# Kernel tuning notes

Hardware: AMD Instinct MI355X
Metric: run time of the kernel (lower is better)

Reference implementation:

```python
import jax, jax.numpy as jnp
import numpy as np

N_WORD = 50000
N_DOC = 10000
E_WW = 800000
E_WD = 320000


def _sage(h_src, h_dst, src, dst, n_dst, W_self, W_neigh, b):
    # DGL SAGEConv('mean'): fc_self(h_dst) + fc_neigh(mean_{u in N(v)} h_u) + bias
    ones = jnp.ones((src.shape[0],), dtype=h_src.dtype)
    deg = jax.ops.segment_sum(ones, dst, num_segments=n_dst)            # [n_dst]
    agg = jax.ops.segment_sum(h_src[src], dst, num_segments=n_dst)      # [n_dst, d]
    mean = agg / jnp.maximum(deg, 1.0)[:, None]                          # zero for isolated
    return h_dst @ W_self + mean @ W_neigh + b


def _layer(xw, xd, edges, Ws, Wn, b):
    (ww_s, ww_d, wwr_s, wwr_d, wd_s, wd_d, wdr_s, wdr_d) = edges
    # relations targeting 'word': word2word, word2wordr, word2documentr
    h_ww = _sage(xw, xw, ww_s, ww_d, N_WORD, Ws[0], Wn[0], b[0])
    h_wwr = _sage(xw, xw, wwr_s, wwr_d, N_WORD, Ws[1], Wn[1], b[1])
    h_wdr = _sage(xd, xw, wdr_s, wdr_d, N_WORD, Ws[3], Wn[3], b[3])
    # relation targeting 'document': word2document
    h_wd = _sage(xw, xd, wd_s, wd_d, N_DOC, Ws[2], Wn[2], b[2])
    # HeteroGraphConv aggregate='stack' then torch.sum(dim=1) == sum over relations; then relu
    return jax.nn.relu(h_ww + h_wwr + h_wdr), jax.nn.relu(h_wd)


def setup_inputs() -> dict:
    key = jax.random.key(0)
    ks = jax.random.split(key, 20)
    d_in, d_h = 256, 128
    inp = {
        "x_word": jax.random.normal(ks[0], (N_WORD, d_in), jnp.float32),
        "x_doc": jax.random.normal(ks[1], (N_DOC, d_in), jnp.float32),
        "ww_src": jax.random.randint(ks[2], (E_WW,), 0, N_WORD, jnp.int32),
        "ww_dst": jax.random.randint(ks[3], (E_WW,), 0, N_WORD, jnp.int32),
        "wwr_src": jax.random.randint(ks[4], (E_WW,), 0, N_WORD, jnp.int32),
        "wwr_dst": jax.random.randint(ks[5], (E_WW,), 0, N_WORD, jnp.int32),
        "wd_src": jax.random.randint(ks[6], (E_WD,), 0, N_WORD, jnp.int32),
        "wd_dst": jax.random.randint(ks[7], (E_WD,), 0, N_DOC, jnp.int32),
        "wdr_src": jax.random.randint(ks[8], (E_WD,), 0, N_DOC, jnp.int32),
        "wdr_dst": jax.random.randint(ks[9], (E_WD,), 0, N_WORD, jnp.int32),
        "Wself1": jax.random.normal(ks[10], (4, d_in, d_h), jnp.float32) * (1.0 / np.sqrt(d_in)),
        "Wneigh1": jax.random.normal(ks[11], (4, d_in, d_h), jnp.float32) * (1.0 / np.sqrt(d_in)),
        "b1": jnp.zeros((4, d_h), jnp.float32),
        "Wself2": jax.random.normal(ks[12], (4, d_h, d_h), jnp.float32) * (1.0 / np.sqrt(d_h)),
        "Wneigh2": jax.random.normal(ks[13], (4, d_h, d_h), jnp.float32) * (1.0 / np.sqrt(d_h)),
        "b2": jnp.zeros((4, d_h), jnp.float32),
        "lin_w": jax.random.normal(ks[14], (1, d_h), jnp.float32) * (1.0 / np.sqrt(d_h)),
        "lin_b": jnp.ones((1,), jnp.float32),
    }
    return inp


def reference(x_word, x_doc, ww_src, ww_dst, wwr_src, wwr_dst, wd_src, wd_dst,
              wdr_src, wdr_dst, Wself1, Wneigh1, b1, Wself2, Wneigh2, b2, lin_w, lin_b):
    edges = (ww_src, ww_dst, wwr_src, wwr_dst, wd_src, wd_dst, wdr_src, wdr_dst)
    xw, xd = _layer(x_word, x_doc, edges, Wself1, Wneigh1, b1)
    xw, xd = _layer(xw, xd, edges, Wself2, Wneigh2, b2)
    out_w = jax.nn.sigmoid(xw @ lin_w.T + lin_b)  # [N_WORD, 1]
    out_d = jax.nn.sigmoid(xd @ lin_w.T + lin_b)  # [N_DOC, 1]
    return out_w, out_d
```

## Files before the change

kernel.cpp:

```cpp
#include <hip/hip_runtime.h>
#include <math.h>

#define N_WORD 50000
#define N_DOC  10000
#define E_WW   800000
#define E_WD   320000
#define D_IN   256
#define D_H    128

#define NPB    256
#define NBK_W  196
#define NBK_D  40
#define BKT    (3 * NBK_W + NBK_D)
#define EPB    8192
#define NBLK_WW 98
#define NBLK_WD 40
#define NBLK_TOT (2 * NBLK_WW + 2 * NBLK_WD)
#define PACK_BLKS 145

#define CAP_WW  4736
#define CAP_WDR 2176
#define CAP_WD  8960

#define WSTRIP ((N_WORD + 63) / 64)
#define DSTRIP ((N_DOC + 63) / 64)
#define NSTRIP (WSTRIP + DSTRIP)

typedef __attribute__((ext_vector_type(8))) short short8;
typedef __attribute__((ext_vector_type(4))) float f32x4;

__device__ inline unsigned short f2bf(float f) {
  unsigned u = __float_as_uint(f);
  u = (u + 0x7fffu + ((u >> 16) & 1u)) >> 16;
  return (unsigned short)u;
}

struct G6 { const short* B[6]; unsigned short* C[6]; };

template <int ABF, int K>
__device__ void gemm_body(const void* __restrict__ Aw, const void* __restrict__ Ad,
                          const G6& g, int blk) {
  constexpr int KT = K >> 5;
  int wid = threadIdx.x >> 6, lane = threadIdx.x & 63;
  const void* A; int M, row0, h0, h1;
  if (blk < WSTRIP) { A = Aw; M = N_WORD; row0 = blk << 6; h0 = 0; h1 = 4; }
  else { A = Ad; M = N_DOC; row0 = (blk - WSTRIP) << 6; h0 = 4; h1 = 6; }
  int r = lane & 15, quad = lane >> 4;
  int m0 = row0 + wid * 16;
  int mA = m0 + r; if (mA >= M) mA = M - 1;
  short8 afr[KT];
  if (ABF) {
    const short* ap = (const short*)A + (size_t)mA * K + quad * 8;
#pragma unroll
    for (int kt = 0; kt < KT; ++kt) afr[kt] = *(const short8*)(ap + kt * 32);
  } else {
    const float* ap = (const float*)A + (size_t)mA * K + quad * 8;
#pragma unroll
    for (int kt = 0; kt < KT; ++kt) {
      float4 a0 = *(const float4*)(ap + kt * 32);
      float4 a1 = *(const float4*)(ap + kt * 32 + 4);
      short8 v;
      v[0] = (short)f2bf(a0.x); v[1] = (short)f2bf(a0.y);
      v[2] = (short)f2bf(a0.z); v[3] = (short)f2bf(a0.w);
      v[4] = (short)f2bf(a1.x); v[5] = (short)f2bf(a1.y);
      v[6] = (short)f2bf(a1.z); v[7] = (short)f2bf(a1.w);
      afr[kt] = v;
    }
  }
  for (int h = h0; h < h1; ++h) {
    const short* Bp = g.B[h];
    f32x4 acc[8];
#pragma unroll
    for (int nt = 0; nt < 8; ++nt) acc[nt] = (f32x4){0.f, 0.f, 0.f, 0.f};
#pragma unroll
    for (int kt = 0; kt < KT; ++kt) {
      const short* bbase = Bp + ((size_t)kt * 4096) + lane * 8;
#pragma unroll
      for (int nt = 0; nt < 8; ++nt) {
        short8 bf = *(const short8*)(bbase + (size_t)nt * 512);
        acc[nt] = __builtin_amdgcn_mfma_f32_16x16x32_bf16(afr[kt], bf, acc[nt], 0, 0, 0);
      }
    }
    unsigned short* C = g.C[h];
#pragma unroll
    for (int nt = 0; nt < 8; ++nt)
#pragma unroll
      for (int rr = 0; rr < 4; ++rr) {
        int row = m0 + quad * 4 + rr;
        if (row < M) C[(size_t)row * 128 + nt * 16 + r] = f2bf(acc[nt][rr]);
      }
  }
}

__global__ __launch_bounds__(256) void prep_kernel(
    const float* __restrict__ Ws1, const float* __restrict__ Wn1,
    const float* __restrict__ Ws2, const float* __restrict__ Wn2,
    short* __restrict__ Bp1, short* __restrict__ Bp2,
    const float* __restrict__ b1, const float* __restrict__ b2,
    float* __restrict__ bs1, float* __restrict__ bs2, int* __restrict__ bcnt) {
  int b = blockIdx.x;
  if (b == PACK_BLKS) {
    for (int i = threadIdx.x; i < BKT; i += 256) bcnt[i] = 0;
    return;
  }
  int tid = b * 256 + threadIdx.x;
  const int L1T = 6 * 4096;
  const int L2T = 6 * 2048;
  if (tid >= L1T + L2T) {
    int t = tid - (L1T + L2T);
    if (t < 128) bs1[t] = b1[t] + b1[128 + t] + b1[384 + t];
    else if (t < 256) { int u = t - 128; bs2[u] = b2[u] + b2[128 + u] + b2[384 + u]; }
    return;
  }
  const float *src0, *src1 = nullptr, *src2 = nullptr;
  short* dstp;
  int kt, nt, lane;
  if (tid < L1T) {
    int mat = tid / 4096, rem = tid % 4096;
    kt = rem / 512; nt = (rem / 64) % 8; lane = rem % 64;
    const int W1 = 256 * 128;
    if (mat == 0) { src0 = Ws1; src1 = Ws1 + W1; src2 = Ws1 + 3 * W1; }
    else if (mat <= 4) src0 = Wn1 + (size_t)(mat - 1) * W1;
    else src0 = Ws1 + 2 * W1;
    dstp = Bp1 + (size_t)mat * W1 + ((size_t)(kt * 8 + nt) * 64 + lane) * 8;
  } else {
    int t2 = tid - L1T;
    int mat = t2 / 2048, rem = t2 % 2048;
    kt = rem / 512; nt = (rem / 64) % 8; lane = rem % 64;
    const int W2 = 128 * 128;
    if (mat == 0) { src0 = Ws2; src1 = Ws2 + W2; src2 = Ws2 + 3 * W2; }
    else if (mat <= 4) src0 = Wn2 + (size_t)(mat - 1) * W2;
    else src0 = Ws2 + 2 * W2;
    dstp = Bp2 + (size_t)mat * W2 + ((size_t)(kt * 8 + nt) * 64 + lane) * 8;
  }
  int n = nt * 16 + (lane & 15);
  int kb = kt * 32 + (lane >> 4) * 8;
  short8 v;
#pragma unroll
  for (int j = 0; j < 8; ++j) {
    float f = src0[(size_t)(kb + j) * 128 + n];
    if (src1) f += src1[(size_t)(kb + j) * 128 + n] + src2[(size_t)(kb + j) * 128 + n];
    v[j] = (short)f2bf(f);
  }
  *(short8*)dstp = v;
}

__device__ inline void rel_map(int b, const int* wwd, const int* wwrd, const int* wdrd,
                               const int* wdd, const int*& dst, int& E, int& gbase, int& lb) {
  if (b < NBLK_WW) { dst = wwd; E = E_WW; gbase = 0; lb = b; }
  else if (b < 2 * NBLK_WW) { dst = wwrd; E = E_WW; gbase = NBK_W; lb = b - NBLK_WW; }
  else if (b < 2 * NBLK_WW + NBLK_WD) { dst = wdrd; E = E_WD; gbase = 2 * NBK_W; lb = b - 2 * NBLK_WW; }
  else { dst = wdd; E = E_WD; gbase = 3 * NBK_W; lb = b - 2 * NBLK_WW - NBLK_WD; }
}

struct BinLDS {
  unsigned buf[EPB];
  int hist[NBK_W];
  int lofs[NBK_W];
  int gofs[NBK_W];
  int lcur[NBK_W];
  int sm[256];
};

__global__ __launch_bounds__(256, 4) void bin_gemm1(
    const int* wws, const int* wwd, const int* wwrs, const int* wwrd,
    const int* wdrs, const int* wdrd, const int* wds, const int* wdd,
    int* bcnt, unsigned* st_ww, unsigned* st_wwr, unsigned* st_wdr, unsigned* st_wd,
    const float* __restrict__ Aw, const float* __restrict__ Ad, G6 g) {
  __shared__ BinLDS L;
  int b = blockIdx.x;
  if (b >= NBLK_TOT) {
    gemm_body<0, 256>(Aw, Ad, g, b - NBLK_TOT);
    return;
  }
  const int* dst; int E, gbase, lb;
  rel_map(b, wwd, wwrd, wdrd, wdd, dst, E, gbase, lb);
  const int* src; unsigned* st; int cap;
  if (b < NBLK_WW) { src = wws; st = st_ww; cap = CAP_WW; }
  else if (b < 2 * NBLK_WW) { src = wwrs; st = st_wwr; cap = CAP_WW; }
  else if (b < 2 * NBLK_WW + NBLK_WD) { src = wdrs; st = st_wdr; cap = CAP_WDR; }
  else { src = wds; st = st_wd; cap = CAP_WD; }
  int tid = threadIdx.x;
  int e0 = lb * EPB;
  int ecnt = E - e0; if (ecnt > EPB) ecnt = EPB;
  if (tid < NBK_W) L.hist[tid] = 0;
  __syncthreads();
  int dcache[EPB / 256];
#pragma unroll
  for (int k = 0; k < EPB / 256; ++k) {
    int i = e0 + k * 256 + tid;
    int d = (i < E) ? dst[i] : -1;
    dcache[k] = d;
    if (d >= 0) atomicAdd(&L.hist[d >> 8], 1);
  }
  __syncthreads();
  {
    int v = (tid < NBK_W) ? L.hist[tid] : 0;
    L.sm[tid] = v;
    __syncthreads();
    for (int o = 1; o < 256; o <<= 1) {
      int add = (tid >= o) ? L.sm[tid - o] : 0;
      __syncthreads();
      L.sm[tid] += add;
      __syncthreads();
    }
    if (tid < NBK_W) {
      int ex = L.sm[tid] - v;
      L.lofs[tid] = ex;
      L.lcur[tid] = ex;
      int base = v ? atomicAdd(&bcnt[gbase + tid], v) : 0;
      L.gofs[tid] = (int)((size_t)tid * cap) + base - ex;
    }
  }
  __syncthreads();
#pragma unroll
  for (int k = 0; k < EPB / 256; ++k) {
    int d = dcache[k];
    if (d >= 0) {
      int i = e0 + k * 256 + tid;
      int bk = d >> 8;
      int p = atomicAdd(&L.lcur[bk], 1);
      L.buf[p] = ((unsigned)bk << 24) | ((unsigned)(d & 255) << 16) |
                 (unsigned)(src[i] & 0xFFFF);
    }
  }
  __syncthreads();
#pragma unroll
  for (int k = 0; k < EPB / 256; ++k) {
    int p = k * 256 + tid;
    if (p < ecnt) {
      unsigned e = L.buf[p];
      st[L.gofs[e >> 24] + p] = e & 0x00FFFFFFu;
    }
  }
}

struct CSRB {
  const unsigned *st_ww, *st_wwr, *st_wdr, *st_wd;
  unsigned short *c_ww, *c_wwr, *c_wdr, *c_wd;
  int *rp_ww, *rp_wwr, *rp_wdr, *rp_wd;
  const int* bcnt;
};

__global__ __launch_bounds__(256) void place_kernel(CSRB q) {
  __shared__ int cnt[256], off[256], sm[256];
  int g = blockIdx.x;
  const unsigned* st; unsigned short* csr; int* rp; int relFirst, relLast, n, cap, Etot;
  if (g < NBK_W)            { st = q.st_ww;  csr = q.c_ww;  rp = q.rp_ww;  relFirst = 0;         relLast = NBK_W - 1;     n = N_WORD; cap = CAP_WW;  Etot = E_WW; }
  else if (g < 2 * NBK_W)   { st = q.st_wwr; csr = q.c_wwr; rp = q.rp_wwr; relFirst = NBK_W;     relLast = 2 * NBK_W - 1; n = N_WORD; cap = CAP_WW;  Etot = E_WW; }
  else if (g < 3 * NBK_W)   { st = q.st_wdr; csr = q.c_wdr; rp = q.rp_wdr; relFirst = 2 * NBK_W; relLast = 3 * NBK_W - 1; n = N_WORD; cap = CAP_WDR; Etot = E_WD; }
  else                      { st = q.st_wd;  csr = q.c_wd;  rp = q.rp_wd;  relFirst = 3 * NBK_W; relLast = BKT - 1;       n = N_DOC;  cap = CAP_WD;  Etot = E_WD; }
  int cb = g - relFirst;
  int tid = threadIdx.x;
  int v = (tid < cb) ? q.bcnt[relFirst + tid] : 0;
  sm[tid] = v;
  __syncthreads();
  for (int o = 128; o > 0; o >>= 1) {
    if (tid < o) sm[tid] += sm[tid + o];
    __syncthreads();
  }
  int bstart = sm[0];
  if (g == relLast && tid == 0) rp[n] = Etot;
  __syncthreads();
  int node_base = cb << 8;
  int node_cnt = n - node_base; if (node_cnt > NPB) node_cnt = NPB;
  int ecnt = q.bcnt[g];
  const unsigned* w = st + (size_t)cb * cap;
  cnt[tid] = 0;
  __syncthreads();
  for (int j = tid; j < ecnt; j += 256) atomicAdd(&cnt[w[j] >> 16], 1);
  __syncthreads();
  int c = cnt[tid];
  sm[tid] = c;
  __syncthreads();
  for (int o = 1; o < 256; o <<= 1) {
    int add = (tid >= o) ? sm[tid - o] : 0;
    __syncthreads();
    sm[tid] += add;
    __syncthreads();
  }
  int ex = sm[tid] - c;
  off[tid] = ex;
  if (tid < node_cnt) rp[node_base + tid] = bstart + ex;
  __syncthreads();
  for (int j = tid; j < ecnt; j += 256) {
    unsigned e = w[j];
    int p = atomicAdd(&off[e >> 16], 1);
    csr[bstart + p] = (unsigned short)(e & 0xFFFFu);
  }
}

__global__ __launch_bounds__(256, 6) void gemm2_kernel(
    const void* __restrict__ Aw, const void* __restrict__ Ad, G6 g) {
  gemm_body<1, 128>(Aw, Ad, g, blockIdx.x);
}

__device__ inline void accum_rel(const unsigned* __restrict__ y,
                                 const unsigned short* __restrict__ csr,
                                 int beg, int end, int lane, float& f0, float& f1) {
  float a0 = 0.f, a1 = 0.f;
  for (int base = beg; base < end; base += 64) {
    int cnt = end - base; if (cnt > 64) cnt = 64;
    int ld = base + lane; if (ld >= end) ld = end - 1;
    int idx = csr[ld];
    int j = 0;
    for (; j + 7 < cnt; j += 8) {
      unsigned u[8];
#pragma unroll
      for (int k = 0; k < 8; ++k) {
        int s = __builtin_amdgcn_readlane(idx, j + k);
        u[k] = y[((size_t)s << 6) + lane];
      }
#pragma unroll
      for (int k = 0; k < 8; ++k) {
        a0 += __uint_as_float(u[k] << 16);
        a1 += __uint_as_float(u[k] & 0xffff0000u);
      }
    }
    for (; j < cnt; ++j) {
      int s = __builtin_amdgcn_readlane(idx, j);
      unsigned uu = y[((size_t)s << 6) + lane];
      a0 += __uint_as_float(uu << 16);
      a1 += __uint_as_float(uu & 0xffff0000u);
    }
  }
  int deg = end - beg;
  float inv = 1.0f / (float)(deg > 1 ? deg : 1);
  f0 += a0 * inv;
  f1 += a1 * inv;
}

__global__ __launch_bounds__(256) void gather_all(
    const unsigned* __restrict__ y_ww, const unsigned* __restrict__ y_wwr,
    const unsigned* __restrict__ y_wdr, const unsigned* __restrict__ y_wd,
    const unsigned short* __restrict__ c_ww, const unsigned short* __restrict__ c_wwr,
    const unsigned short* __restrict__ c_wdr, const unsigned short* __restrict__ c_wd,
    const int* __restrict__ r_ww, const int* __restrict__ r_wwr,
    const int* __restrict__ r_wdr, const int* __restrict__ r_wd,
    const unsigned* __restrict__ tW, const unsigned* __restrict__ tD,
    const float* __restrict__ bW, const float* __restrict__ bD,
    const float* __restrict__ lw, const float* __restrict__ lb,
    unsigned* __restrict__ oW16, unsigned* __restrict__ oD16,
    float* __restrict__ oF, int mode) {
  int gn = (blockIdx.x << 2) + (threadIdx.x >> 6);
  if (gn >= N_WORD + N_DOC) return;
  int lane = threadIdx.x & 63;
  float f0, f1;
  if (gn < N_WORD) {
    int node = gn;
    unsigned tu = tW[((size_t)node << 6) + lane];
    f0 = __uint_as_float(tu << 16);
    f1 = __uint_as_float(tu & 0xffff0000u);
    accum_rel(y_ww, c_ww, r_ww[node], r_ww[node + 1], lane, f0, f1);
    accum_rel(y_wwr, c_wwr, r_wwr[node], r_wwr[node + 1], lane, f0, f1);
    accum_rel(y_wdr, c_wdr, r_wdr[node], r_wdr[node + 1], lane, f0, f1);
    float2 bv = ((const float2*)bW)[lane];
    f0 = fmaxf(f0 + bv.x, 0.f);
    f1 = fmaxf(f1 + bv.y, 0.f);
    if (mode == 1) {
      oW16[((size_t)node << 6) + lane] = (unsigned)f2bf(f0) | ((unsigned)f2bf(f1) << 16);
    } else {
      float2 lv = ((const float2*)lw)[lane];
      float s = f0 * lv.x + f1 * lv.y;
#pragma unroll
      for (int off = 32; off > 0; off >>= 1) s += __shfl_xor(s, off);
      if (lane == 0) oF[node] = 1.0f / (1.0f + expf(-(s + lb[0])));
    }
  } else {
    int node = gn - N_WORD;
    unsigned tu = tD[((size_t)node << 6) + lane];
    f0 = __uint_as_float(tu << 16);
    f1 = __uint_as_float(tu & 0xffff0000u);
    accum_rel(y_wd, c_wd, r_wd[node], r_wd[node + 1], lane, f0, f1);
    float2 bv = ((const float2*)bD)[lane];
    f0 = fmaxf(f0 + bv.x, 0.f);
    f1 = fmaxf(f1 + bv.y, 0.f);
    if (mode == 1) {
      oD16[((size_t)node << 6) + lane] = (unsigned)f2bf(f0) | ((unsigned)f2bf(f1) << 16);
    } else {
      float2 lv = ((const float2*)lw)[lane];
      float s = f0 * lv.x + f1 * lv.y;
#pragma unroll
      for (int off = 32; off > 0; off >>= 1) s += __shfl_xor(s, off);
      if (lane == 0) oF[N_WORD + node] = 1.0f / (1.0f + expf(-(s + lb[0])));
    }
  }
}

extern "C" void kernel_launch(void* const* d_in, const int* in_sizes, int n_in,
                              void* d_out, int out_size, void* d_ws, size_t ws_size,
                              hipStream_t stream) {
  const float* xw      = (const float*)d_in[0];
  const float* xd      = (const float*)d_in[1];
  const int*   ww_src  = (const int*)d_in[2];
  const int*   ww_dst  = (const int*)d_in[3];
  const int*   wwr_src = (const int*)d_in[4];
  const int*   wwr_dst = (const int*)d_in[5];
  const int*   wd_src  = (const int*)d_in[6];
  const int*   wd_dst  = (const int*)d_in[7];
  const int*   wdr_src = (const int*)d_in[8];
  const int*   wdr_dst = (const int*)d_in[9];
  const float* Ws1     = (const float*)d_in[10];
  const float* Wn1     = (const float*)d_in[11];
  const float* b1      = (const float*)d_in[12];
  const float* Ws2     = (const float*)d_in[13];
  const float* Wn2     = (const float*)d_in[14];
  const float* b2      = (const float*)d_in[15];
  const float* lin_w   = (const float*)d_in[16];
  const float* lin_b   = (const float*)d_in[17];
  float* out = (float*)d_out;

  char* p = (char*)d_ws;
  auto alloc = [&](size_t nbytes) {
    char* r = p;
    p += (nbytes + 255) & ~(size_t)255;
    return r;
  };
  unsigned* twA  = (unsigned*)alloc((size_t)N_WORD * D_H * 2);
  unsigned* tdA  = (unsigned*)alloc((size_t)N_DOC * D_H * 2);
  unsigned* xw1B = (unsigned*)alloc((size_t)N_WORD * D_H * 2);
  unsigned* xd1B = (unsigned*)alloc((size_t)N_DOC * D_H * 2);
  unsigned* yB0 = (unsigned*)alloc((size_t)N_WORD * D_H * 2);
  unsigned* yB1 = (unsigned*)alloc((size_t)N_WORD * D_H * 2);
  unsigned* yB2 = (unsigned*)alloc((size_t)N_WORD * D_H * 2);
  unsigned* ydB = (unsigned*)alloc((size_t)N_DOC * D_H * 2);
  unsigned short* csr_ww  = (unsigned short*)alloc((size_t)E_WW * 2);
  unsigned short* csr_wwr = (unsigned short*)alloc((size_t)E_WW * 2);
  unsigned short* csr_wdr = (unsigned short*)alloc((size_t)E_WD * 2);
  unsigned short* csr_wd  = (unsigned short*)alloc((size_t)E_WD * 2);
  int* rp_ww  = (int*)alloc((size_t)(N_WORD + 1) * 4);
  int* rp_wwr = (int*)alloc((size_t)(N_WORD + 1) * 4);
  int* rp_wdr = (int*)alloc((size_t)(N_WORD + 1) * 4);
  int* rp_wd  = (int*)alloc((size_t)(N_DOC + 1) * 4);
  short* Bp1 = (short*)alloc((size_t)6 * 256 * 128 * 2);
  short* Bp2 = (short*)alloc((size_t)6 * 128 * 128 * 2);
  int* bcnt  = (int*)alloc((size_t)BKT * 4);
  float* bs1 = (float*)alloc(D_H * 4);
  float* bs2 = (float*)alloc(D_H * 4);
  unsigned* yBX = (unsigned*)alloc((size_t)N_WORD * D_H * 2);
  unsigned* st_ww  = yB0;
  unsigned* st_wwr = st_ww + (size_t)NBK_W * CAP_WW;
  unsigned* st_wdr = yB1;
  unsigned* st_wd  = st_wdr + (size_t)NBK_W * CAP_WDR;

  const int W1 = 256 * 128;
  const int W2 = 128 * 128;

  prep_kernel<<<PACK_BLKS + 1, 256, 0, stream>>>(
      Ws1, Wn1, Ws2, Wn2, Bp1, Bp2, b1, b2, bs1, bs2, bcnt);

  G6 g1;
  g1.B[0] = Bp1 + 0 * W1; g1.C[0] = (unsigned short*)twA;
  g1.B[1] = Bp1 + 1 * W1; g1.C[1] = (unsigned short*)yB2;
  g1.B[2] = Bp1 + 2 * W1; g1.C[2] = (unsigned short*)xw1B;
  g1.B[3] = Bp1 + 3 * W1; g1.C[3] = (unsigned short*)yBX;
  g1.B[4] = Bp1 + 5 * W1; g1.C[4] = (unsigned short*)tdA;
  g1.B[5] = Bp1 + 4 * W1; g1.C[5] = (unsigned short*)ydB;
  bin_gemm1<<<NBLK_TOT + NSTRIP, 256, 0, stream>>>(
      ww_src, ww_dst, wwr_src, wwr_dst, wdr_src, wdr_dst, wd_src, wd_dst,
      bcnt, st_ww, st_wwr, st_wdr, st_wd, xw, xd, g1);

  CSRB q;
  q.st_ww = st_ww; q.st_wwr = st_wwr; q.st_wdr = st_wdr; q.st_wd = st_wd;
  q.c_ww = csr_ww; q.c_wwr = csr_wwr; q.c_wdr = csr_wdr; q.c_wd = csr_wd;
  q.rp_ww = rp_ww; q.rp_wwr = rp_wwr; q.rp_wdr = rp_wdr; q.rp_wd = rp_wd;
  q.bcnt = bcnt;
  place_kernel<<<BKT, 256, 0, stream>>>(q);

  gather_all<<<(N_WORD + N_DOC + 3) / 4, 256, 0, stream>>>(
      yB2, xw1B, ydB, yBX, csr_ww, csr_wwr, csr_wdr, csr_wd,
      rp_ww, rp_wwr, rp_wdr, rp_wd, twA, tdA, bs1, b1 + 256,
      lin_w, lin_b, yB0, xd1B, nullptr, 1);

  G6 g2;
  g2.B[0] = Bp2 + 0 * W2; g2.C[0] = (unsigned short*)twA;
  g2.B[1] = Bp2 + 1 * W2; g2.C[1] = (unsigned short*)yB2;
  g2.B[2] = Bp2 + 2 * W2; g2.C[2] = (unsigned short*)xw1B;
  g2.B[3] = Bp2 + 3 * W2; g2.C[3] = (unsigned short*)yBX;
  g2.B[4] = Bp2 + 5 * W2; g2.C[4] = (unsigned short*)tdA;
  g2.B[5] = Bp2 + 4 * W2; g2.C[5] = (unsigned short*)ydB;
  gemm2_kernel<<<NSTRIP, 256, 0, stream>>>(yB0, xd1B, g2);

  gather_all<<<(N_WORD + N_DOC + 3) / 4, 256, 0, stream>>>(
      yB2, xw1B, ydB, yBX, csr_ww, csr_wwr, csr_wdr, csr_wd,
      rp_ww, rp_wwr, rp_wdr, rp_wd, twA, tdA, bs2, b2 + 256,
      lin_w, lin_b, nullptr, nullptr, out, 2);
}
```

Before: 400.5 us.

## Gather four neighbor rows per wave with 16-byte loads and a zero pad row

The neighbor-mean gather now has each wave split into four 16-lane groups. Each group fetches a different neighbor row with uint4 loads, and the partial sums are combined with cross-group shuffles at the end. Out-of-range slots point to an extra zeroed padding row appended to each feature buffer, so the loop needs no scalar tail. This is meant to raise memory-level parallelism and cut load instruction count in the gather, which dominates the kernel. In exchange it adds shuffle reductions and reshuffles the workspace buffer sizes, which risks aliasing with the staging buffers.

```diff
diff --git a/kernel.cpp b/kernel.cpp
--- a/kernel.cpp
+++ b/kernel.cpp
@@ -34,6 +34,9 @@
   u = (u + 0x7fffu + ((u >> 16) & 1u)) >> 16;
   return (unsigned short)u;
 }
+
+__device__ inline float bflo(unsigned u) { return __uint_as_float(u << 16); }
+__device__ inline float bfhi(unsigned u) { return __uint_as_float(u & 0xffff0000u); }
 
 struct G6 { const short* B[6]; unsigned short* C[6]; };
 
@@ -97,10 +100,18 @@
     const float* __restrict__ Ws2, const float* __restrict__ Wn2,
     short* __restrict__ Bp1, short* __restrict__ Bp2,
     const float* __restrict__ b1, const float* __restrict__ b2,
-    float* __restrict__ bs1, float* __restrict__ bs2, int* __restrict__ bcnt) {
+    float* __restrict__ bs1, float* __restrict__ bs2, int* __restrict__ bcnt,
+    unsigned* __restrict__ zA, unsigned* __restrict__ zB,
+    unsigned* __restrict__ zC, unsigned* __restrict__ zD) {
   int b = blockIdx.x;
   if (b == PACK_BLKS) {
     for (int i = threadIdx.x; i < BKT; i += 256) bcnt[i] = 0;
+    if (threadIdx.x < 64) {
+      zA[(size_t)N_WORD * 64 + threadIdx.x] = 0;
+      zB[(size_t)N_WORD * 64 + threadIdx.x] = 0;
+      zC[(size_t)N_WORD * 64 + threadIdx.x] = 0;
+      zD[(size_t)N_DOC * 64 + threadIdx.x] = 0;
+    }
     return;
   }
   int tid = b * 256 + threadIdx.x;
@@ -295,39 +306,41 @@
   gemm_body<1, 128>(Aw, Ad, g, blockIdx.x);
 }
 
-__device__ inline void accum_rel(const unsigned* __restrict__ y,
-                                 const unsigned short* __restrict__ csr,
-                                 int beg, int end, int lane, float& f0, float& f1) {
-  float a0 = 0.f, a1 = 0.f;
+__device__ inline void accum_rel4(const uint4* __restrict__ Y,
+                                  const unsigned short* __restrict__ csr,
+                                  int beg, int end, int lane, int r, int g,
+                                  int zrow, float* __restrict__ f) {
+  int deg = end - beg;
+  if (deg <= 0) return;
+  float a[8];
+#pragma unroll
+  for (int i = 0; i < 8; ++i) a[i] = 0.f;
   for (int base = beg; base < end; base += 64) {
     int cnt = end - base; if (cnt > 64) cnt = 64;
     int ld = base + lane; if (ld >= end) ld = end - 1;
     int idx = csr[ld];
-    int j = 0;
-    for (; j + 7 < cnt; j += 8) {
-      unsigned u[8];
-#pragma unroll
-      for (int k = 0; k < 8; ++k) {
-        int s = __builtin_amdgcn_readlane(idx, j + k);
-        u[k] = y[((size_t)s << 6) + lane];
+    for (int j = 0; j < cnt; j += 16) {
+      uint4 u[4];
+#pragma unroll
+      for (int t = 0; t < 4; ++t) {
+        int e = j + (t << 2) + g;
+        int sel = (e < cnt) ? e : 0;
+        int sv = __shfl(idx, sel, 64);
+        int s = (e < cnt) ? sv : zrow;
+        u[t] = Y[(unsigned)((s << 4) + r)];
       }
 #pragma unroll
-      for (int k = 0; k < 8; ++k) {
-        a0 += __uint_as_float(u[k] << 16);
-        a1 += __uint_as_float(u[k] & 0xffff0000u);
+      for (int t = 0; t < 4; ++t) {
+        a[0] += bflo(u[t].x); a[1] += bfhi(u[t].x);
+        a[2] += bflo(u[t].y); a[3] += bfhi(u[t].y);
+        a[4] += bflo(u[t].z); a[5] += bfhi(u[t].z);
+        a[6] += bflo(u[t].w); a[7] += bfhi(u[t].w);
       }
     }
-    for (; j < cnt; ++j) {
-      int s = __builtin_amdgcn_readlane(idx, j);
-      unsigned uu = y[((size_t)s << 6) + lane];
-      a0 += __uint_as_float(uu << 16);
-      a1 += __uint_as_float(uu & 0xffff0000u);
-    }
-  }
-  int deg = end - beg;
-  float inv = 1.0f / (float)(deg > 1 ? deg : 1);
-  f0 += a0 * inv;
-  f1 += a1 * inv;
+  }
+  float inv = 1.0f / (float)deg;
+#pragma unroll
+  for (int i = 0; i < 8; ++i) f[i] += a[i] * inv;
 }
 
 __global__ __launch_bounds__(256) void gather_all(
@@ -345,45 +358,55 @@
   int gn = (blockIdx.x << 2) + (threadIdx.x >> 6);
   if (gn >= N_WORD + N_DOC) return;
   int lane = threadIdx.x & 63;
-  float f0, f1;
-  if (gn < N_WORD) {
-    int node = gn;
-    unsigned tu = tW[((size_t)node << 6) + lane];
-    f0 = __uint_as_float(tu << 16);
-    f1 = __uint_as_float(tu & 0xffff0000u);
-    accum_rel(y_ww, c_ww, r_ww[node], r_ww[node + 1], lane, f0, f1);
-    accum_rel(y_wwr, c_wwr, r_wwr[node], r_wwr[node + 1], lane, f0, f1);
-    accum_rel(y_wdr, c_wdr, r_wdr[node], r_wdr[node + 1], lane, f0, f1);
-    float2 bv = ((const float2*)bW)[lane];
-    f0 = fmaxf(f0 + bv.x, 0.f);
-    f1 = fmaxf(f1 + bv.y, 0.f);
-    if (mode == 1) {
-      oW16[((size_t)node << 6) + lane] = (unsigned)f2bf(f0) | ((unsigned)f2bf(f1) << 16);
-    } else {
-      float2 lv = ((const float2*)lw)[lane];
-      float s = f0 * lv.x + f1 * lv.y;
-#pragma unroll
-      for (int off = 32; off > 0; off >>= 1) s += __shfl_xor(s, off);
-      if (lane == 0) oF[node] = 1.0f / (1.0f + expf(-(s + lb[0])));
-    }
+  int r = lane & 15, g = lane >> 4;
+  float f[8];
+#pragma unroll
+  for (int i = 0; i < 8; ++i) f[i] = 0.f;
+  bool isw = (gn < N_WORD);
+  int node = isw ? gn : gn - N_WORD;
+  if (isw) {
+    accum_rel4((const uint4*)y_ww, c_ww, r_ww[node], r_ww[node + 1], lane, r, g, N_WORD, f);
+    accum_rel4((const uint4*)y_wwr, c_wwr, r_wwr[node], r_wwr[node + 1], lane, r, g, N_WORD, f);
+    accum_rel4((const uint4*)y_wdr, c_wdr, r_wdr[node], r_wdr[node + 1], lane, r, g, N_DOC, f);
   } else {
-    int node = gn - N_WORD;
-    unsigned tu = tD[((size_t)node << 6) + lane];
-    f0 = __uint_as_float(tu << 16);
-    f1 = __uint_as_float(tu & 0xffff0000u);
-    accum_rel(y_wd, c_wd, r_wd[node], r_wd[node + 1], lane, f0, f1);
-    float2 bv = ((const float2*)bD)[lane];
-    f0 = fmaxf(f0 + bv.x, 0.f);
-    f1 = fmaxf(f1 + bv.y, 0.f);
-    if (mode == 1) {
-      oD16[((size_t)node << 6) + lane] = (unsigned)f2bf(f0) | ((unsigned)f2bf(f1) << 16);
-    } else {
-      float2 lv = ((const float2*)lw)[lane];
-      float s = f0 * lv.x + f1 * lv.y;
-#pragma unroll
-      for (int off = 32; off > 0; off >>= 1) s += __shfl_xor(s, off);
-      if (lane == 0) oF[N_WORD + node] = 1.0f / (1.0f + expf(-(s + lb[0])));
-    }
+    accum_rel4((const uint4*)y_wd, c_wd, r_wd[node], r_wd[node + 1], lane, r, g, N_WORD, f);
+  }
+#pragma unroll
+  for (int i = 0; i < 8; ++i) {
+    f[i] += __shfl_xor(f[i], 16, 64);
+    f[i] += __shfl_xor(f[i], 32, 64);
+  }
+  const unsigned* tS = isw ? tW : tD;
+  uint4 tu = ((const uint4*)tS)[(unsigned)((node << 4) + r)];
+  const float* bs = isw ? bW : bD;
+  float4 bv0 = ((const float4*)bs)[2 * r];
+  float4 bv1 = ((const float4*)bs)[2 * r + 1];
+  f[0] = fmaxf(f[0] + bflo(tu.x) + bv0.x, 0.f);
+  f[1] = fmaxf(f[1] + bfhi(tu.x) + bv0.y, 0.f);
+  f[2] = fmaxf(f[2] + bflo(tu.y) + bv0.z, 0.f);
+  f[3] = fmaxf(f[3] + bfhi(tu.y) + bv0.w, 0.f);
+  f[4] = fmaxf(f[4] + bflo(tu.z) + bv1.x, 0.f);
+  f[5] = fmaxf(f[5] + bfhi(tu.z) + bv1.y, 0.f);
+  f[6] = fmaxf(f[6] + bflo(tu.w) + bv1.z, 0.f);
+  f[7] = fmaxf(f[7] + bfhi(tu.w) + bv1.w, 0.f);
+  if (mode == 1) {
+    if (g == 0) {
+      uint4 pk;
+      pk.x = (unsigned)f2bf(f[0]) | ((unsigned)f2bf(f[1]) << 16);
+      pk.y = (unsigned)f2bf(f[2]) | ((unsigned)f2bf(f[3]) << 16);
+      pk.z = (unsigned)f2bf(f[4]) | ((unsigned)f2bf(f[5]) << 16);
+      pk.w = (unsigned)f2bf(f[6]) | ((unsigned)f2bf(f[7]) << 16);
+      unsigned* o = isw ? oW16 : oD16;
+      ((uint4*)o)[(unsigned)((node << 4) + r)] = pk;
+    }
+  } else {
+    float4 lv0 = ((const float4*)lw)[2 * r];
+    float4 lv1 = ((const float4*)lw)[2 * r + 1];
+    float s = f[0] * lv0.x + f[1] * lv0.y + f[2] * lv0.z + f[3] * lv0.w +
+              f[4] * lv1.x + f[5] * lv1.y + f[6] * lv1.z + f[7] * lv1.w;
+#pragma unroll
+    for (int off = 8; off > 0; off >>= 1) s += __shfl_xor(s, off, 64);
+    if (lane == 0) oF[isw ? node : N_WORD + node] = 1.0f / (1.0f + expf(-(s + lb[0])));
   }
 }
 
@@ -418,12 +441,12 @@
   };
   unsigned* twA  = (unsigned*)alloc((size_t)N_WORD * D_H * 2);
   unsigned* tdA  = (unsigned*)alloc((size_t)N_DOC * D_H * 2);
-  unsigned* xw1B = (unsigned*)alloc((size_t)N_WORD * D_H * 2);
+  unsigned* xw1B = (unsigned*)alloc((size_t)N_WORD * D_H * 2 + 256);
   unsigned* xd1B = (unsigned*)alloc((size_t)N_DOC * D_H * 2);
   unsigned* yB0 = (unsigned*)alloc((size_t)N_WORD * D_H * 2);
-  unsigned* yB1 = (unsigned*)alloc((size_t)N_WORD * D_H * 2);
-  unsigned* yB2 = (unsigned*)alloc((size_t)N_WORD * D_H * 2);
-  unsigned* ydB = (unsigned*)alloc((size_t)N_DOC * D_H * 2);
+  unsigned* yB1 = (unsigned*)alloc(((size_t)NBK_W * CAP_WDR + (size_t)NBK_D * CAP_WD) * 4);
+  unsigned* yB2 = (unsigned*)alloc((size_t)N_WORD * D_H * 2 + 256);
+  unsigned* ydB = (unsigned*)alloc((size_t)N_DOC * D_H * 2 + 256);
   unsigned short* csr_ww  = (unsigned short*)alloc((size_t)E_WW * 2);
   unsigned short* csr_wwr = (unsigned short*)alloc((size_t)E_WW * 2);
   unsigned short* csr_wdr = (unsigned short*)alloc((size_t)E_WD * 2);
@@ -437,7 +460,7 @@
   int* bcnt  = (int*)alloc((size_t)BKT * 4);
   float* bs1 = (float*)alloc(D_H * 4);
   float* bs2 = (float*)alloc(D_H * 4);
-  unsigned* yBX = (unsigned*)alloc((size_t)N_WORD * D_H * 2);
+  unsigned* yBX = (unsigned*)alloc((size_t)N_WORD * D_H * 2 + 256);
   unsigned* st_ww  = yB0;
   unsigned* st_wwr = st_ww + (size_t)NBK_W * CAP_WW;
   unsigned* st_wdr = yB1;
@@ -447,7 +470,8 @@
   const int W2 = 128 * 128;
 
   prep_kernel<<<PACK_BLKS + 1, 256, 0, stream>>>(
-      Ws1, Wn1, Ws2, Wn2, Bp1, Bp2, b1, b2, bs1, bs2, bcnt);
+      Ws1, Wn1, Ws2, Wn2, Bp1, Bp2, b1, b2, bs1, bs2, bcnt,
+      yB2, xw1B, yBX, ydB);
 
   G6 g1;
   g1.B[0] = Bp1 + 0 * W1; g1.C[0] = (unsigned short*)twA;
```

Result: faster. 385.8 us (-3.7%).
